# Kernel tuning notes

Hardware: AMD Instinct MI355X
Metric: run time of the kernel (lower is better)

Reference implementation:

```python
import jax, jax.numpy as jnp
import numpy as np

HS = 64      # head_size
MS = 2048    # memory_size
NH = 4       # num_heads
H = 512      # hidden_size


def setup_inputs() -> dict:
    key = jax.random.key(0)
    ks = jax.random.split(key, 6)
    B, T, I, O = 32, 32, 256, 256
    ctrl_in = I + NH * HS  # 512

    def p(k, shape, fan):
        return jax.random.normal(k, shape, jnp.float32) / np.sqrt(fan).astype(np.float32)

    return {
        "x": jax.random.normal(ks[0], (B, T, I), jnp.float32),
        "W_ih": p(ks[1], (4 * H, ctrl_in), ctrl_in),
        "W_hh": p(ks[2], (4 * H, H), H),
        "b_ih": jnp.zeros((4 * H,), jnp.float32),
        "b_hh": jnp.zeros((4 * H,), jnp.float32),
        "W_head": p(ks[3], (NH * (HS + MS + 3), H), H),
        "b_head": jnp.zeros((NH * (HS + MS + 3),), jnp.float32),
        "W_out": p(ks[4], (O, H + NH * HS), H + NH * HS),
        "b_out": jnp.zeros((O,), jnp.float32),
    }


def reference(x, W_ih, W_hh, b_ih, b_hh, W_head, b_head, W_out, b_out):
    B, T, _ = x.shape
    scale = 1.0 / np.sqrt(HS).astype(np.float32)

    def step(carry, x_t):
        h, c, mem, read = carry
        # controller LSTM cell (PyTorch gate order i,f,g,o)
        inp = jnp.concatenate([x_t, read.reshape(B, -1)], axis=-1)
        gates = inp @ W_ih.T + b_ih + h @ W_hh.T + b_hh
        i, f, g, o = jnp.split(gates, 4, axis=-1)
        c = jax.nn.sigmoid(f) * c + jax.nn.sigmoid(i) * jnp.tanh(g)
        h = jax.nn.sigmoid(o) * jnp.tanh(c)
        # head params: [B, NH, HS + MS + 3]
        hp = (h @ W_head.T + b_head).reshape(B, NH, HS + MS + 3)
        # read addressing (uses memory BEFORE write)
        read_keys = hp[:, :, :HS]
        rw = jax.nn.softmax(jnp.einsum('bnk,bmk->bnm', read_keys, mem) * scale, axis=-1)
        read = jnp.einsum('bnm,bmh->bnh', rw, mem)
        # write addressing
        write_keys = hp[:, :, HS:2 * HS]
        write_strength = jax.nn.sigmoid(hp[:, :, 2 * HS:2 * HS + 1])
        ww = jax.nn.softmax(jnp.einsum('bnk,bmk->bnm', write_keys, mem) * scale, axis=-1)
        mem = mem + jnp.einsum('bnm,bnh->bmh', ww, write_strength * write_keys)
        # output projection
        out = jnp.concatenate([h, read.reshape(B, -1)], axis=-1) @ W_out.T + b_out
        return (h, c, mem, read), out

    h0 = jnp.zeros((B, H), x.dtype)
    c0 = jnp.zeros((B, H), x.dtype)
    mem0 = jnp.zeros((B, MS, HS), x.dtype)
    read0 = jnp.zeros((B, NH, HS), x.dtype)
    (h, c, mem, _), outs = jax.lax.scan(step, (h0, c0, mem0, read0), jnp.swapaxes(x, 0, 1))
    outputs = jnp.swapaxes(outs, 0, 1)  # [B, T, O]
    return outputs, mem, (h, c)
```

## Files before the change

kernel.cpp:

```cpp
#include <hip/hip_runtime.h>
#include <math.h>

#define B 32
#define T 32
#define O_DIM 256
#define H_DIM 512
#define HS 64
#define MS 2048
#define NCOL 516
#define NCH 32

typedef __attribute__((ext_vector_type(4))) float f4;

__device__ __forceinline__ float sigm(float x){ return 1.0f/(1.0f+__expf(-x)); }
__device__ __forceinline__ float hsum(f4 v){ return (v.x + v.y) + (v.z + v.w); }

__global__ __launch_bounds__(256) void k_transpose_t(float* __restrict__ dst,
                                                     const float* __restrict__ src,
                                                     int N, int K){
  __shared__ float tile[32][33];
  int jb = blockIdx.x*32, kb = blockIdx.y*32;
  int tj = threadIdx.x & 31, tk = threadIdx.x >> 5;
  #pragma unroll
  for (int p = 0; p < 4; ++p){
    int j = jb + tk + p*8, k = kb + tj;
    if (j < N && k < K) tile[tk + p*8][tj] = src[j*K + k];
  }
  __syncthreads();
  #pragma unroll
  for (int p = 0; p < 4; ++p){
    int k = kb + tk + p*8, j = jb + tj;
    if (j < N && k < K) dst[k*N + j] = tile[tj][tk + p*8];
  }
}

__global__ __launch_bounds__(256) void k_ghead(float* __restrict__ dst,
                                               const float* __restrict__ W_head){
  int idx = blockIdx.x*256 + threadIdx.x;
  if (idx >= 520*512) return;
  int col = idx >> 9, k = idx & 511;
  float v = 0.f;
  if (col < NCOL){ int n = col/129, c = col%129; v = W_head[((size_t)n*2115 + c)*512 + k]; }
  dst[idx] = v;
}

__global__ __launch_bounds__(256) void k_xt(f4* __restrict__ XT4,
                                            const float* __restrict__ x){
  int idx = blockIdx.x*256 + threadIdx.x;
  int b = idx & 31, k4 = (idx >> 5) & 63, t = idx >> 11;
  XT4[idx] = ((const f4*)x)[(size_t)(b*T + t)*64 + k4];
}

__global__ __launch_bounds__(512) void k_A(
    const f4* __restrict__ XT4, const float* __restrict__ W_ih,
    const float* __restrict__ W_hh, const float* __restrict__ b_ih,
    const float* __restrict__ b_hh, const f4* __restrict__ READT4,
    float* __restrict__ HHT, float* __restrict__ CF, int t)
{
  __shared__ f4 WS[8*256];
  __shared__ float glp[2][8][33];
  const int bid = blockIdx.x, tid = threadIdx.x;
  const f4* HHT4 = (const f4*)HHT;
  for (int idx = tid; idx < 2048; idx += 512){
    int rsub = idx >> 8, q = idx & 255;
    int gate = rsub & 3, jj = (rsub >> 2) & 1;
    int row = gate*512 + bid*2 + jj;
    WS[idx] = (q < 128) ? ((const f4*)W_ih)[(size_t)row*128 + q]
                        : ((const f4*)W_hh)[(size_t)row*128 + (q - 128)];
  }
  __syncthreads();
  {
    int b = tid & 31, rsub = (tid >> 5) & 7, khalf = tid >> 8;
    const f4* w = WS + rsub*256;
    f4 a0 = {0.f,0.f,0.f,0.f}, a1 = {0.f,0.f,0.f,0.f};
    if (khalf == 0){
      const f4* xt4 = XT4 + (size_t)t*2048;
      #pragma unroll 4
      for (int k4 = 0; k4 < 64; k4 += 2){
        a0 += w[k4]     * xt4[k4*32 + b];
        a1 += w[k4+1]   * xt4[(k4+1)*32 + b];
      }
      #pragma unroll 4
      for (int k4 = 0; k4 < 64; k4 += 2){
        a0 += w[64+k4]   * READT4[k4*32 + b];
        a1 += w[64+k4+1] * READT4[(k4+1)*32 + b];
      }
    } else if (t > 0){
      const f4* ht4 = HHT4 + (size_t)(t-1)*4096;
      #pragma unroll 4
      for (int k4 = 0; k4 < 128; k4 += 2){
        a0 += w[128+k4]   * ht4[k4*32 + b];
        a1 += w[128+k4+1] * ht4[(k4+1)*32 + b];
      }
    }
    glp[khalf][rsub][b] = hsum(a0 + a1);
  }
  __syncthreads();
  if (tid < 64){
    int b2 = tid & 31, jj2 = tid >> 5;
    int j2 = bid*2 + jj2;
    int r0 = 0*512 + j2, r1 = 1*512 + j2, r2 = 2*512 + j2, r3 = 3*512 + j2;
    float gi = glp[0][jj2*4+0][b2] + glp[1][jj2*4+0][b2] + b_ih[r0] + b_hh[r0];
    float gf = glp[0][jj2*4+1][b2] + glp[1][jj2*4+1][b2] + b_ih[r1] + b_hh[r1];
    float gg = glp[0][jj2*4+2][b2] + glp[1][jj2*4+2][b2] + b_ih[r2] + b_hh[r2];
    float go = glp[0][jj2*4+3][b2] + glp[1][jj2*4+3][b2] + b_ih[r3] + b_hh[r3];
    float c = sigm(gf)*CF[b2*512+j2] + sigm(gi)*tanhf(gg);
    float h = sigm(go)*tanhf(c);
    CF[b2*512+j2] = c;
    HHT[((size_t)t*128 + (j2>>2))*128 + b2*4 + (j2&3)] = h;
  }
}

__global__ __launch_bounds__(256) void k_B(
    const float* __restrict__ HHT, const float* __restrict__ WT_HD2,
    const float* __restrict__ b_head, float* __restrict__ HPT, int t)
{
  __shared__ float red[256];
  const int bid = blockIdx.x, tid = threadIdx.x;
  const f4* HHT4 = (const f4*)HHT;
  int b = tid & 31, cs = (tid>>5)&1, kq = tid>>6;
  int col = bid*2 + cs;
  const f4* hT4 = HHT4 + (size_t)t*4096 + kq*1024;
  const f4* w4  = (const f4*)(WT_HD2 + (size_t)col*512) + kq*32;
  f4 acc4 = {0.f, 0.f, 0.f, 0.f};
  #pragma unroll 4
  for (int k4 = 0; k4 < 32; ++k4)
    acc4 += w4[k4] * hT4[k4*32 + b];
  red[tid] = hsum(acc4);
  __syncthreads();
  if (kq == 0){
    float v = red[tid] + red[tid + 64] + red[tid + 128] + red[tid + 192];
    if (col < NCOL){ int n = col/129, c = col%129; v += b_head[n*2115 + c]; }
    HPT[col*32 + b] = v;
  }
}

__global__ __launch_bounds__(512) void k_CD(
    float* __restrict__ MEM, const float* __restrict__ HPT,
    float* __restrict__ SW, float* __restrict__ PART, float* __restrict__ PREAD,
    const float* __restrict__ WST, const float* __restrict__ WKS, int t)
{
  __shared__ float keys[8][64];
  __shared__ float mc[2][64][68];
  __shared__ float sc[2][4][64];
  __shared__ float ew[2][4][64];
  __shared__ f4 wkp[4][16];
  __shared__ float gmp[4], facp[4];
  const int bid = blockIdx.x, tid = threadIdx.x;
  f4* MEM4 = (f4*)MEM;
  int xcd = bid & 7, t2 = bid >> 3;
  int b = xcd*4 + (t2 & 3), ch8 = t2 >> 2;
  int hkh = tid >> 8, tl = tid & 255;
  if (tid < 512){
    int kk = tid >> 6, e = tid & 63;
    int n = kk & 3;
    int c = (kk >= 4) ? (64 + e) : e;
    keys[kk][e] = HPT[(n*129 + c)*32 + b];
  }
  if (t > 0){
    if (tid < 64){
      int n = tid >> 4, e4 = tid & 15;
      wkp[n][e4] = ((const f4*)WKS)[(b*4 + n)*16 + e4];
    }
    if (tid < 4){ gmp[tid] = WST[b*8 + tid*2]; facp[tid] = WST[b*8 + tid*2 + 1]; }
  }
  for (int sub = 0; sub < 2; ++sub){
    int ch = ch8*4 + hkh*2 + sub;
    __syncthreads();
    for (int idx = tl; idx < 64*16; idx += 256){
      int m = idx >> 4, e4 = idx & 15;
      ((f4*)&mc[hkh][m][0])[e4] = MEM4[((size_t)b*MS + ch*64 + m)*16 + e4];
    }
    if (t > 0){
      int n = tl >> 6, m = tl & 63;
      float s = SW[((size_t)b*4 + n)*MS + ch*64 + m];
      ew[hkh][n][m] = __expf(s - gmp[n]) * facp[n];
    }
    __syncthreads();
    if (t > 0){
      for (int idx = tl; idx < 1024; idx += 256){
        int m = idx >> 4, e4 = idx & 15;
        f4 v = ((f4*)&mc[hkh][m][0])[e4];
        v += ew[hkh][0][m]*wkp[0][e4] + ew[hkh][1][m]*wkp[1][e4]
           + ew[hkh][2][m]*wkp[2][e4] + ew[hkh][3][m]*wkp[3][e4];
        ((f4*)&mc[hkh][m][0])[e4] = v;
        MEM4[((size_t)b*MS + ch*64 + m)*16 + e4] = v;
      }
      __syncthreads();
    }
    {
      int m = tl & 63, kp = tl >> 6;
      const f4* mrow4 = (const f4*)&mc[hkh][m][0];
      int k0 = kp*2, k1 = kp*2+1;
      f4 s0v = {0.f,0.f,0.f,0.f}, s1v = {0.f,0.f,0.f,0.f};
      #pragma unroll 4
      for (int e4 = 0; e4 < 16; ++e4){
        f4 mv = mrow4[e4];
        s0v += mv * (*(const f4*)&keys[k0][e4*4]);
        s1v += mv * (*(const f4*)&keys[k1][e4*4]);
      }
      float s0 = hsum(s0v)*0.125f, s1 = hsum(s1v)*0.125f;
      if (kp >= 2){
        float* swp = SW + ((size_t)b*4 + (k0-4))*MS + ch*64 + m;
        swp[0] = s0; swp[MS] = s1;
      }
      float mx0 = s0, mx1 = s1;
      #pragma unroll
      for (int off = 32; off > 0; off >>= 1){
        mx0 = fmaxf(mx0, __shfl_xor(mx0, off, 64));
        mx1 = fmaxf(mx1, __shfl_xor(mx1, off, 64));
      }
      float e0 = __expf(s0 - mx0), e1 = __expf(s1 - mx1);
      float sm0 = e0, sm1 = e1;
      #pragma unroll
      for (int off = 32; off > 0; off >>= 1){
        sm0 += __shfl_xor(sm0, off, 64);
        sm1 += __shfl_xor(sm1, off, 64);
      }
      if (kp < 2){ sc[hkh][k0][m] = e0; sc[hkh][k1][m] = e1; }
      if (m == 0){
        float* pp = PART + (((size_t)b*NCH + ch)*8 + k0)*2;
        pp[0] = mx0; pp[1] = sm0;
        pp[2] = mx1; pp[3] = sm1;
      }
    }
    __syncthreads();
    {
      int n = tl >> 6, e = tl & 63;
      float pr = 0.f;
      for (int m = 0; m < 64; ++m) pr += sc[hkh][n][m] * mc[hkh][m][e];
      PREAD[(((size_t)b*NCH + ch)*4 + n)*64 + e] = pr;
    }
  }
}

__global__ __launch_bounds__(256) void k_Dlite(
    const float* __restrict__ HPT, const float* __restrict__ PART,
    const float* __restrict__ PREAD, float* __restrict__ READT,
    float* __restrict__ RHIST, float* __restrict__ WST, float* __restrict__ WKS,
    const float* __restrict__ HHT, float* __restrict__ HF, int t)
{
  __shared__ float gm2[4], dn2[4];
  const int bid = blockIdx.x, tid = threadIdx.x;
  const f4* HHT4 = (const f4*)HHT;
  int b = bid;
  if (tid < 4){
    int kk = 4 + tid;
    const float* pp = PART + ((size_t)b*NCH*8 + kk)*2;
    float mx = -1e30f;
    for (int ch = 0; ch < NCH; ++ch) mx = fmaxf(mx, pp[ch*16]);
    float d = 0.f;
    for (int ch = 0; ch < NCH; ++ch) d += pp[ch*16+1]*__expf(pp[ch*16] - mx);
    float st = sigm(HPT[(tid*129 + 128)*32 + b]);
    WST[b*8 + tid*2]     = mx;
    WST[b*8 + tid*2 + 1] = st / d;
  }
  {
    int n = tid >> 6, e = tid & 63;
    WKS[(b*4 + n)*64 + e] = HPT[(n*129 + 64 + e)*32 + b];
  }
  if (tid < 4){
    const float* pp = PART + ((size_t)b*NCH*8 + tid)*2;
    float mx = -1e30f;
    for (int ch = 0; ch < NCH; ++ch) mx = fmaxf(mx, pp[ch*16]);
    float d = 0.f;
    for (int ch = 0; ch < NCH; ++ch) d += pp[ch*16+1]*__expf(pp[ch*16] - mx);
    gm2[tid] = mx; dn2[tid] = d;
  }
  __syncthreads();
  {
    int n = tid >> 6, e = tid & 63;
    float gmn = gm2[n], dnn = dn2[n];
    float r = 0.f;
    for (int ch = 0; ch < NCH; ++ch){
      float cm = PART[(((size_t)b*NCH + ch)*8 + n)*2];
      r += PREAD[(((size_t)b*NCH + ch)*4 + n)*64 + e] * __expf(cm - gmn);
    }
    r /= dnn;
    int k = n*64 + e;
    READT[(k>>2)*128 + b*4 + (k&3)] = r;
    RHIST[((size_t)t*64 + (k>>2))*128 + b*4 + (k&3)] = r;
  }
  if (t == T-1){
    int i = bid*256 + tid;
    if (i < 4096){
      int j4 = i & 127, bb = i >> 7;
      ((f4*)HF)[i] = HHT4[((size_t)(T-1)*128 + j4)*32 + bb];
    }
  }
}

__global__ __launch_bounds__(256) void k_flush(
    float* __restrict__ MEM, const float* __restrict__ SW,
    const float* __restrict__ WST, const float* __restrict__ WKS)
{
  __shared__ float gm[4], fac[4];
  __shared__ f4 wk4[4][16];
  __shared__ float ew[4][256];
  const int bid = blockIdx.x, tid = threadIdx.x;
  int xcd = bid & 7, t2 = bid >> 3;
  int b = xcd*4 + (t2 & 3), sub = t2 >> 2;
  if (tid < 4){ gm[tid] = WST[b*8 + tid*2]; fac[tid] = WST[b*8 + tid*2 + 1]; }
  if (tid < 64){
    int n = tid >> 4, e4 = tid & 15;
    wk4[n][e4] = ((const f4*)WKS)[(b*4 + n)*16 + e4];
  }
  __syncthreads();
  for (int idx = tid; idx < 1024; idx += 256){
    int n = idx >> 8, m = idx & 255;
    float s = SW[((size_t)b*4 + n)*MS + sub*256 + m];
    ew[n][m] = __expf(s - gm[n]) * fac[n];
  }
  __syncthreads();
  {
    int e4 = tid & 15, ms = tid >> 4;
    f4 k0 = wk4[0][e4], k1 = wk4[1][e4], k2 = wk4[2][e4], k3 = wk4[3][e4];
    #pragma unroll 2
    for (int it = 0; it < 16; ++it){
      int m = it*16 + ms;
      float w0 = ew[0][m], w1 = ew[1][m];
      float w2 = ew[2][m], w3 = ew[3][m];
      f4* p = (f4*)MEM + ((size_t)b*MS + sub*256 + m)*16 + e4;
      f4 v = *p;
      v += w0*k0 + w1*k1 + w2*k2 + w3*k3;
      *p = v;
    }
  }
}

__global__ __launch_bounds__(256) void k_out(
    const float* __restrict__ HHT, const float* __restrict__ RHIST,
    const float* __restrict__ WT_OUT, const float* __restrict__ b_out,
    float* __restrict__ out)
{
  __shared__ float A[16][260];
  const int bid = blockIdx.x, tid = threadIdx.x;
  const f4* HHT4 = (const f4*)HHT;
  const f4* RHIST4 = (const f4*)RHIST;
  const f4* W4 = (const f4*)WT_OUT;
  int nt = bid & 3, mt = bid >> 2;
  int rl = tid & 15, og = tid >> 4;
  int o = nt*64 + og*4, o4 = o >> 2;
  f4 a0 = {0.f,0.f,0.f,0.f}, a1 = a0, a2 = a0, a3 = a0;
  for (int kc = 0; kc < 3; ++kc){
    __syncthreads();
    for (int idx = tid; idx < 1024; idx += 256){
      int r = idx >> 6, k4 = idx & 63;
      int row = mt*16 + r;
      int bb = row >> 5, tt = row & 31;
      int kg4 = kc*64 + k4;
      f4 v = (kg4 < 128)
        ? HHT4[((size_t)tt*128 + kg4)*32 + bb]
        : RHIST4[((size_t)tt*64 + (kg4-128))*32 + bb];
      *(f4*)&A[r][k4*4] = v;
    }
    __syncthreads();
    const float* Ar = &A[rl][0];
    const f4* wp = W4 + (size_t)kc*256*64 + o4;
    #pragma unroll 2
    for (int k = 0; k < 256; k += 4){
      a0 += Ar[k]   * wp[(size_t)(k)*64];
      a1 += Ar[k+1] * wp[(size_t)(k+1)*64];
      a2 += Ar[k+2] * wp[(size_t)(k+2)*64];
      a3 += Ar[k+3] * wp[(size_t)(k+3)*64];
    }
  }
  int row = mt*16 + rl;
  f4 accv = (a0 + a1) + (a2 + a3);
  accv += *(const f4*)(b_out + o);
  *(f4*)(out + (size_t)row*O_DIM + o) = accv;
}

extern "C" void kernel_launch(void* const* d_in, const int* in_sizes, int n_in,
                              void* d_out, int out_size, void* d_ws, size_t ws_size,
                              hipStream_t stream)
{
  const float* x      = (const float*)d_in[0];
  const float* W_ih   = (const float*)d_in[1];
  const float* W_hh   = (const float*)d_in[2];
  const float* b_ih   = (const float*)d_in[3];
  const float* b_hh   = (const float*)d_in[4];
  const float* W_head = (const float*)d_in[5];
  const float* b_head = (const float*)d_in[6];
  const float* W_out  = (const float*)d_in[7];
  const float* b_out  = (const float*)d_in[8];

  float* out = (float*)d_out;
  float* MEM = out + B*T*O_DIM;
  float* HF  = MEM + (size_t)B*MS*HS;
  float* CF  = HF + B*H_DIM;

  float* ws      = (float*)d_ws;
  float* WT_HD2  = ws;
  float* WT_OUT  = WT_HD2 + 520*512;
  float* XT      = WT_OUT + 768*256;
  float* SW      = XT     + 262144;
  float* PART    = SW     + 262144;
  float* PREAD   = PART   + 16384;
  float* HPT     = PREAD  + 262144;
  float* READT   = HPT    + 16640;
  float* HHT     = READT  + 8192;
  float* RHIST   = HHT    + 524288;
  float* WST     = RHIST  + 262144;
  float* WKS     = WST    + 256;

  (void)hipMemsetAsync(MEM, 0, ((size_t)B*MS*HS + 2*B*H_DIM)*sizeof(float), stream);
  (void)hipMemsetAsync(READT, 0, (size_t)8192*sizeof(float), stream);

  k_ghead<<<1040, 256, 0, stream>>>(WT_HD2, W_head);
  k_transpose_t<<<dim3(8, 24), 256, 0, stream>>>(WT_OUT, W_out, 256, 768);
  k_xt<<<256, 256, 0, stream>>>((f4*)XT, x);

  for (int t = 0; t < T; ++t){
    k_A<<<256, 512, 0, stream>>>((const f4*)XT, W_ih, W_hh, b_ih, b_hh,
                                 (const f4*)READT, HHT, CF, t);
    k_B<<<260, 256, 0, stream>>>(HHT, WT_HD2, b_head, HPT, t);
    k_CD<<<256, 512, 0, stream>>>(MEM, HPT, SW, PART, PREAD, WST, WKS, t);
    k_Dlite<<<32, 256, 0, stream>>>(HPT, PART, PREAD, READT, RHIST, WST, WKS,
                                    HHT, HF, t);
  }
  k_flush<<<256, 256, 0, stream>>>(MEM, SW, WST, WKS);
  k_out<<<256, 256, 0, stream>>>(HHT, RHIST, WT_OUT, b_out, out);
}
```

Baseline: 1.210 ms.

## Fuse read-reduction kernel into memory kernel via last-block atomic counter

Merges the per-step k_Dlite reduction into k_CD. Each batch's 8 chunk blocks increment an atomic counter, and the last-arriving block does the softmax merge, read computation and write-state setup, then resets the counter. This removes one kernel launch and its inter-kernel gap per timestep. In exchange it adds release/acquire fences and atomics, and the final reduction runs serialized in one block per batch.

```diff
diff --git a/kernel.cpp b/kernel.cpp
--- a/kernel.cpp
+++ b/kernel.cpp
@@ -135,10 +135,13 @@
   }
 }
 
-__global__ __launch_bounds__(512) void k_CD(
+__global__ __launch_bounds__(512) void k_CDD(
     float* __restrict__ MEM, const float* __restrict__ HPT,
     float* __restrict__ SW, float* __restrict__ PART, float* __restrict__ PREAD,
-    const float* __restrict__ WST, const float* __restrict__ WKS, int t)
+    float* __restrict__ WST, float* __restrict__ WKS,
+    float* __restrict__ READT, float* __restrict__ RHIST,
+    const float* __restrict__ HHT, float* __restrict__ HF,
+    unsigned* __restrict__ DCNT, int t)
 {
   __shared__ float keys[8][64];
   __shared__ float mc[2][64][68];
@@ -146,6 +149,8 @@
   __shared__ float ew[2][4][64];
   __shared__ f4 wkp[4][16];
   __shared__ float gmp[4], facp[4];
+  __shared__ float gm2[4], dn2[4];
+  __shared__ int lastf;
   const int bid = blockIdx.x, tid = threadIdx.x;
   f4* MEM4 = (f4*)MEM;
   int xcd = bid & 7, t2 = bid >> 3;
@@ -232,62 +237,64 @@
       PREAD[(((size_t)b*NCH + ch)*4 + n)*64 + e] = pr;
     }
   }
-}
-
-__global__ __launch_bounds__(256) void k_Dlite(
-    const float* __restrict__ HPT, const float* __restrict__ PART,
-    const float* __restrict__ PREAD, float* __restrict__ READT,
-    float* __restrict__ RHIST, float* __restrict__ WST, float* __restrict__ WKS,
-    const float* __restrict__ HHT, float* __restrict__ HF, int t)
-{
-  __shared__ float gm2[4], dn2[4];
-  const int bid = blockIdx.x, tid = threadIdx.x;
-  const f4* HHT4 = (const f4*)HHT;
-  int b = bid;
+
+  __syncthreads();
+  if (tid == 0){
+    __builtin_amdgcn_fence(__ATOMIC_RELEASE, "agent");
+    unsigned old = __hip_atomic_fetch_add(&DCNT[b], 1u, __ATOMIC_RELAXED,
+                                          __HIP_MEMORY_SCOPE_AGENT);
+    lastf = (old == 7u);
+    if (old == 7u) __builtin_amdgcn_fence(__ATOMIC_ACQUIRE, "agent");
+  }
+  __syncthreads();
+  if (!lastf) return;
+
   if (tid < 4){
     int kk = 4 + tid;
     const float* pp = PART + ((size_t)b*NCH*8 + kk)*2;
     float mx = -1e30f;
-    for (int ch = 0; ch < NCH; ++ch) mx = fmaxf(mx, pp[ch*16]);
+    for (int c2 = 0; c2 < NCH; ++c2) mx = fmaxf(mx, pp[c2*16]);
     float d = 0.f;
-    for (int ch = 0; ch < NCH; ++ch) d += pp[ch*16+1]*__expf(pp[ch*16] - mx);
+    for (int c2 = 0; c2 < NCH; ++c2) d += pp[c2*16+1]*__expf(pp[c2*16] - mx);
     float st = sigm(HPT[(tid*129 + 128)*32 + b]);
     WST[b*8 + tid*2]     = mx;
     WST[b*8 + tid*2 + 1] = st / d;
   }
-  {
+  if (tid < 256){
     int n = tid >> 6, e = tid & 63;
     WKS[(b*4 + n)*64 + e] = HPT[(n*129 + 64 + e)*32 + b];
   }
   if (tid < 4){
     const float* pp = PART + ((size_t)b*NCH*8 + tid)*2;
     float mx = -1e30f;
-    for (int ch = 0; ch < NCH; ++ch) mx = fmaxf(mx, pp[ch*16]);
+    for (int c2 = 0; c2 < NCH; ++c2) mx = fmaxf(mx, pp[c2*16]);
     float d = 0.f;
-    for (int ch = 0; ch < NCH; ++ch) d += pp[ch*16+1]*__expf(pp[ch*16] - mx);
+    for (int c2 = 0; c2 < NCH; ++c2) d += pp[c2*16+1]*__expf(pp[c2*16] - mx);
     gm2[tid] = mx; dn2[tid] = d;
   }
   __syncthreads();
-  {
+  if (tid < 256){
     int n = tid >> 6, e = tid & 63;
     float gmn = gm2[n], dnn = dn2[n];
     float r = 0.f;
-    for (int ch = 0; ch < NCH; ++ch){
-      float cm = PART[(((size_t)b*NCH + ch)*8 + n)*2];
-      r += PREAD[(((size_t)b*NCH + ch)*4 + n)*64 + e] * __expf(cm - gmn);
+    for (int c2 = 0; c2 < NCH; ++c2){
+      float cm = PART[(((size_t)b*NCH + c2)*8 + n)*2];
+      r += PREAD[(((size_t)b*NCH + c2)*4 + n)*64 + e] * __expf(cm - gmn);
     }
     r /= dnn;
     int k = n*64 + e;
     READT[(k>>2)*128 + b*4 + (k&3)] = r;
     RHIST[((size_t)t*64 + (k>>2))*128 + b*4 + (k&3)] = r;
   }
-  if (t == T-1){
-    int i = bid*256 + tid;
+  if (t == T-1 && tid < 256){
+    int i = b*256 + tid;
     if (i < 4096){
       int j4 = i & 127, bb = i >> 7;
-      ((f4*)HF)[i] = HHT4[((size_t)(T-1)*128 + j4)*32 + bb];
-    }
-  }
+      ((f4*)HF)[i] = ((const f4*)HHT)[((size_t)(T-1)*128 + j4)*32 + bb];
+    }
+  }
+  if (tid == 0)
+    __hip_atomic_store(&DCNT[b], 0u, __ATOMIC_RELAXED, __HIP_MEMORY_SCOPE_AGENT);
 }
 
 __global__ __launch_bounds__(256) void k_flush(
@@ -399,13 +406,14 @@
   float* PREAD   = PART   + 16384;
   float* HPT     = PREAD  + 262144;
   float* READT   = HPT    + 16640;
-  float* HHT     = READT  + 8192;
+  unsigned* DCNT = (unsigned*)(READT + 8192);
+  float* HHT     = READT  + 8192 + 32;
   float* RHIST   = HHT    + 524288;
   float* WST     = RHIST  + 262144;
   float* WKS     = WST    + 256;
 
   (void)hipMemsetAsync(MEM, 0, ((size_t)B*MS*HS + 2*B*H_DIM)*sizeof(float), stream);
-  (void)hipMemsetAsync(READT, 0, (size_t)8192*sizeof(float), stream);
+  (void)hipMemsetAsync(READT, 0, (size_t)(8192 + 32)*sizeof(float), stream);
 
   k_ghead<<<1040, 256, 0, stream>>>(WT_HD2, W_head);
   k_transpose_t<<<dim3(8, 24), 256, 0, stream>>>(WT_OUT, W_out, 256, 768);
@@ -415,9 +423,8 @@
     k_A<<<256, 512, 0, stream>>>((const f4*)XT, W_ih, W_hh, b_ih, b_hh,
                                  (const f4*)READT, HHT, CF, t);
     k_B<<<260, 256, 0, stream>>>(HHT, WT_HD2, b_head, HPT, t);
-    k_CD<<<256, 512, 0, stream>>>(MEM, HPT, SW, PART, PREAD, WST, WKS, t);
-    k_Dlite<<<32, 256, 0, stream>>>(HPT, PART, PREAD, READT, RHIST, WST, WKS,
-                                    HHT, HF, t);
+    k_CDD<<<256, 512, 0, stream>>>(MEM, HPT, SW, PART, PREAD, WST, WKS,
+                                   READT, RHIST, HHT, HF, DCNT, t);
   }
   k_flush<<<256, 256, 0, stream>>>(MEM, SW, WST, WKS);
   k_out<<<256, 256, 0, stream>>>(HHT, RHIST, WT_OUT, b_out, out);
```

Measured after the change: 1.291 ms. 6.7% more time.
